# Kernel tuning notes

Measured on AMD Instinct MI355X. Metric: run time of the kernel, lower is better.

The kernel has to match this reference:

```python
import jax, jax.numpy as jnp
import numpy as np

D_MODEL, D_FF, N_EXPERTS, TOP_K = 1024, 2048, 8, 2
B, S = 2, 2048

def setup_inputs() -> dict:
    key = jax.random.key(0)
    k1, k2, k3, k4 = jax.random.split(key, 4)
    scale = 0.02
    return {
        "x": jax.random.normal(k1, (B, S, D_MODEL), dtype=jnp.float32),
        "gate_w": jax.random.normal(k2, (D_MODEL, N_EXPERTS), dtype=jnp.float32) * scale,
        "w1": jax.random.normal(k3, (N_EXPERTS, D_MODEL, D_FF), dtype=jnp.float32) * scale,
        "w2": jax.random.normal(k4, (N_EXPERTS, D_FF, D_MODEL), dtype=jnp.float32) * scale,
    }

def reference(x, gate_w, w1, w2):
    # --- Router (eval mode: no exploration noise, no dropout) ---
    router_logits = jnp.einsum('bsd,de->bse', x, gate_w)          # [B,S,E]
    top_logits, top_idx = jax.lax.top_k(router_logits, TOP_K)      # [B,S,K]
    top_w = jax.nn.softmax(top_logits, axis=-1)                    # [B,S,K]
    # topk indices are distinct per token, so per-(token,expert) combine weight
    # is the sum over k of weight_k * 1[idx_k == e] (matches torch gather/argmax logic)
    combine = jnp.sum(
        jax.nn.one_hot(top_idx, N_EXPERTS, dtype=x.dtype) * top_w[..., None],
        axis=-2)                                                   # [B,S,E]
    # --- Experts: dense-compute formulation of the gather/MLP/scatter loop ---
    h = jax.nn.silu(jnp.einsum('bsd,edf->ebsf', x, w1))            # [E,B,S,Dff]
    y = jnp.einsum('ebsf,efd->ebsd', h, w2)                        # [E,B,S,D]
    out = jnp.einsum('ebsd,bse->bsd', y, combine)                  # [B,S,D]
    return out
```

## Files before the change

### kernel.cpp

```cpp
#include <hip/hip_runtime.h>
#include <cstdint>
#include <cstddef>

#define D_MODEL 1024
#define D_FF    2048
#define N_EXP   8
#define NTOK    4096
#define NASSIGN (NTOK * 2)

typedef __bf16 bf16_t;
typedef bf16_t bf16x8 __attribute__((ext_vector_type(8)));
typedef float  f32x4  __attribute__((ext_vector_type(4)));

typedef __attribute__((address_space(3))) void       lds_void;
typedef const __attribute__((address_space(1))) void gl_void;

__device__ __forceinline__ unsigned short f2b(float f) {
  union { float f; unsigned u; } v; v.f = f;
  unsigned u = v.u;
  unsigned r = (u + 0x7FFFu + ((u >> 16) & 1u)) >> 16;
  return (unsigned short)r;
}
__device__ __forceinline__ float b2f(unsigned short b) {
  union { unsigned u; float f; } v; v.u = ((unsigned)b) << 16; return v.f;
}

__global__ __launch_bounds__(256) void router_k(
    const float* __restrict__ x, const float* __restrict__ gw,
    int* __restrict__ eidx, float* __restrict__ ewt)
{
  const int wv = threadIdx.x >> 6, lane = threadIdx.x & 63;
  const int token = blockIdx.x * 4 + wv;
  const float4* xr4 = (const float4*)(x + (size_t)token * D_MODEL);
  const float4* gw4 = (const float4*)gw;

  float acc[8] = {};
  #pragma unroll
  for (int it = 0; it < 4; ++it) {
    float4 xv = xr4[it * 64 + lane];
    int d0 = it * 256 + lane * 4;
    #pragma unroll
    for (int i = 0; i < 4; ++i) {
      int d = d0 + i;
      float4 g0 = gw4[d * 2];
      float4 g1 = gw4[d * 2 + 1];
      float xs = (i == 0) ? xv.x : (i == 1) ? xv.y : (i == 2) ? xv.z : xv.w;
      acc[0] += xs * g0.x; acc[1] += xs * g0.y;
      acc[2] += xs * g0.z; acc[3] += xs * g0.w;
      acc[4] += xs * g1.x; acc[5] += xs * g1.y;
      acc[6] += xs * g1.z; acc[7] += xs * g1.w;
    }
  }
  #pragma unroll
  for (int m = 1; m < 64; m <<= 1) {
    #pragma unroll
    for (int k = 0; k < 8; ++k) acc[k] += __shfl_xor(acc[k], m);
  }
  if (lane == 0) {
    int i1 = 0; float v1 = acc[0];
    #pragma unroll
    for (int k = 1; k < 8; ++k) if (acc[k] > v1) { v1 = acc[k]; i1 = k; }
    int i2 = -1; float v2 = -1e30f;
    #pragma unroll
    for (int k = 0; k < 8; ++k) if (k != i1 && acc[k] > v2) { v2 = acc[k]; i2 = k; }
    float t  = __expf(v2 - v1);
    float w1 = 1.f / (1.f + t);
    float w2 = t * w1;
    eidx[token * 2 + 0] = i1; eidx[token * 2 + 1] = i2;
    ewt [token * 2 + 0] = w1; ewt [token * 2 + 1] = w2;
  }
}

__global__ __launch_bounds__(256) void scan_k(
    const int* __restrict__ eidx, const float* __restrict__ ewt,
    int* __restrict__ counts, int* __restrict__ offsets,
    int* __restrict__ rowtok, float* __restrict__ rowwt, int* __restrict__ rowof)
{
  __shared__ int hist[256][9];
  __shared__ int soff[8];
  const int t = threadIdx.x;

  int local[8] = {};
  #pragma unroll 4
  for (int i = 0; i < 32; ++i) local[eidx[t * 32 + i]]++;
  #pragma unroll
  for (int e = 0; e < 8; ++e) hist[t][e] = local[e];
  __syncthreads();

  for (int ofs = 1; ofs < 256; ofs <<= 1) {
    int v[8];
    if (t >= ofs) {
      #pragma unroll
      for (int e = 0; e < 8; ++e) v[e] = hist[t - ofs][e];
    }
    __syncthreads();
    if (t >= ofs) {
      #pragma unroll
      for (int e = 0; e < 8; ++e) hist[t][e] += v[e];
    }
    __syncthreads();
  }

  if (t == 0) {
    int o = 0;
    for (int e = 0; e < 8; ++e) {
      int c = hist[255][e];
      counts[e] = c;
      offsets[e] = o;
      soff[e] = o;
      o += c;
    }
  }
  __syncthreads();

  int run[8];
  #pragma unroll
  for (int e = 0; e < 8; ++e) run[e] = soff[e] + hist[t][e] - local[e];

  #pragma unroll 4
  for (int i = 0; i < 32; ++i) {
    int b = t * 32 + i;
    int e = eidx[b];
    int row = run[e]++;
    rowtok[row] = b >> 1;
    rowwt[row]  = ewt[b];
    rowof[b]    = row;
  }
}

__global__ __launch_bounds__(256) void gather_k(
    const float* __restrict__ x, const int* __restrict__ rowtok,
    unsigned short* __restrict__ Xe)
{
  const int row = blockIdx.x;
  const int token = rowtok[row];
  const float4* xr = (const float4*)(x + (size_t)token * D_MODEL);
  ushort4* dst = (ushort4*)(Xe + (size_t)row * D_MODEL);
  float4 v = xr[threadIdx.x];
  ushort4 o;
  o.x = f2b(v.x); o.y = f2b(v.y); o.z = f2b(v.z); o.w = f2b(v.w);
  dst[threadIdx.x] = o;
}

__global__ __launch_bounds__(256) void transcvt_k(
    const float* __restrict__ in, unsigned short* __restrict__ out, int R, int C)
{
  __shared__ float T[64][65];
  const int e = blockIdx.z;
  const float* ein = in + (size_t)e * R * C;
  unsigned short* eout = out + (size_t)e * R * C;
  const int c0 = blockIdx.x * 64, r0 = blockIdx.y * 64;
  const int g = threadIdx.x >> 4;
  const int m = threadIdx.x & 15;

  #pragma unroll
  for (int i = 0; i < 4; ++i) {
    int r = i * 16 + g;
    float4 v = *(const float4*)(ein + (size_t)(r0 + r) * C + c0 + m * 4);
    T[r][m * 4 + 0] = v.x; T[r][m * 4 + 1] = v.y;
    T[r][m * 4 + 2] = v.z; T[r][m * 4 + 3] = v.w;
  }
  __syncthreads();
  #pragma unroll
  for (int i = 0; i < 4; ++i) {
    int c = i * 16 + g;
    ushort4 o;
    o.x = f2b(T[m * 4 + 0][c]); o.y = f2b(T[m * 4 + 1][c]);
    o.z = f2b(T[m * 4 + 2][c]); o.w = f2b(T[m * 4 + 3][c]);
    *(ushort4*)(eout + (size_t)(c0 + c) * R + r0 + m * 4) = o;
  }
}

template<int K, int N, int MODE>
__global__ __launch_bounds__(256) void moe_gemm_k(
    const unsigned short* __restrict__ A,
    const unsigned short* __restrict__ Bt,
    unsigned short* __restrict__ Hout,
    const int* __restrict__ counts, const int* __restrict__ offsets,
    const float* __restrict__ rowwt)
{
  const int e = blockIdx.z;
  const int cnt = counts[e];
  const int m0 = blockIdx.y * 128;
  if (m0 >= cnt) return;
  const int base = offsets[e];
  const int n0 = blockIdx.x * 128;

  __shared__ unsigned short lA[128 * 32];
  __shared__ unsigned short lB[128 * 32];

  const int tid = threadIdx.x;
  const int lane = tid & 63;
  const int wv = tid >> 6;
  const int wm = wv & 1, wn = wv >> 1;
  const int col = lane & 15, quad = lane >> 4;

  const unsigned short* Aseg = A + (size_t)base * K;
  const unsigned short* Bseg = Bt + (size_t)e * ((size_t)N * K);

  f32x4 acc[4][4] = {};

  for (int k0 = 0; k0 < K; k0 += 32) {
    __syncthreads();
    #pragma unroll
    for (int r = 0; r < 2; ++r) {
      int flat = ((r * 4 + wv) * 64 + lane) * 16;
      int row = flat >> 6;
      int kb  = flat & 63;
      const char* gA = (const char*)Aseg + ((size_t)(m0 + row) * K + k0) * 2 + kb;
      const char* gB = (const char*)Bseg + ((size_t)(n0 + row) * K + k0) * 2 + kb;
      char* lpa = (char*)lA + (r * 4 + wv) * 1024;
      char* lpb = (char*)lB + (r * 4 + wv) * 1024;
      __builtin_amdgcn_global_load_lds((gl_void*)gA, (lds_void*)lpa, 16, 0, 0);
      __builtin_amdgcn_global_load_lds((gl_void*)gB, (lds_void*)lpb, 16, 0, 0);
    }
    __syncthreads();

    bf16x8 af[4], bfr[4];
    #pragma unroll
    for (int i = 0; i < 4; ++i)
      af[i] = *(const bf16x8*)(lA + ((wm * 64 + i * 16 + col) * 32 + quad * 8));
    #pragma unroll
    for (int j = 0; j < 4; ++j)
      bfr[j] = *(const bf16x8*)(lB + ((wn * 64 + j * 16 + col) * 32 + quad * 8));
    #pragma unroll
    for (int i = 0; i < 4; ++i)
      #pragma unroll
      for (int j = 0; j < 4; ++j)
        acc[i][j] = __builtin_amdgcn_mfma_f32_16x16x32_bf16(af[i], bfr[j], acc[i][j], 0, 0, 0);
  }

  #pragma unroll
  for (int i = 0; i < 4; ++i) {
    #pragma unroll
    for (int reg = 0; reg < 4; ++reg) {
      int r = m0 + wm * 64 + i * 16 + quad * 4 + reg;
      if (r < cnt) {
        unsigned short* hrow = Hout + (size_t)(base + r) * N + (n0 + wn * 64 + col);
        if (MODE == 1) {
          #pragma unroll
          for (int j = 0; j < 4; ++j) {
            float v = acc[i][j][reg];
            float s = v / (1.f + __expf(-v));
            hrow[j * 16] = f2b(s);
          }
        } else {
          float wgt = rowwt[base + r];
          #pragma unroll
          for (int j = 0; j < 4; ++j)
            hrow[j * 16] = f2b(wgt * acc[i][j][reg]);
        }
      }
    }
  }
}

__global__ __launch_bounds__(256) void combine_k(
    const unsigned short* __restrict__ Y, const int* __restrict__ rowof,
    float* __restrict__ out)
{
  const int token = blockIdx.x;
  const int r1 = rowof[token * 2];
  const int r2 = rowof[token * 2 + 1];
  const int d4 = threadIdx.x;
  ushort4 a = *(const ushort4*)(Y + (size_t)r1 * D_MODEL + d4 * 4);
  ushort4 b = *(const ushort4*)(Y + (size_t)r2 * D_MODEL + d4 * 4);
  float4 o;
  o.x = b2f(a.x) + b2f(b.x);
  o.y = b2f(a.y) + b2f(b.y);
  o.z = b2f(a.z) + b2f(b.z);
  o.w = b2f(a.w) + b2f(b.w);
  *(float4*)(out + (size_t)token * D_MODEL + d4 * 4) = o;
}

extern "C" void kernel_launch(void* const* d_in, const int* in_sizes, int n_in,
                              void* d_out, int out_size, void* d_ws, size_t ws_size,
                              hipStream_t stream) {
  const float* x  = (const float*)d_in[0];
  const float* gw = (const float*)d_in[1];
  const float* w1 = (const float*)d_in[2];
  const float* w2 = (const float*)d_in[3];
  float* out = (float*)d_out;

  char* ws = (char*)d_ws;
  size_t off = 0;
  auto alloc = [&](size_t bytes) -> char* {
    char* p = ws + off; off += (bytes + 255) & ~(size_t)255; return p;
  };
  int*   ctrl    = (int*)alloc(256);
  int*   counts  = ctrl;
  int*   offsets = ctrl + 8;
  int*   eidx    = (int*)  alloc((size_t)NASSIGN * 4);
  float* ewt     = (float*)alloc((size_t)NASSIGN * 4);
  int*   rowtok  = (int*)  alloc((size_t)NASSIGN * 4);
  float* rowwt   = (float*)alloc((size_t)NASSIGN * 4);
  int*   rowof   = (int*)  alloc((size_t)NASSIGN * 4);
  unsigned short* Xe  = (unsigned short*)alloc((size_t)(NASSIGN + 128) * D_MODEL * 2);
  unsigned short* H   = (unsigned short*)alloc((size_t)(NASSIGN + 128) * D_FF * 2);
  unsigned short* Y   = (unsigned short*)alloc((size_t)(NASSIGN + 128) * D_MODEL * 2);
  unsigned short* w1t = (unsigned short*)alloc((size_t)N_EXP * D_MODEL * D_FF * 2);
  unsigned short* w2t = (unsigned short*)alloc((size_t)N_EXP * D_MODEL * D_FF * 2);

  router_k<<<NTOK / 4, 256, 0, stream>>>(x, gw, eidx, ewt);
  scan_k<<<1, 256, 0, stream>>>(eidx, ewt, counts, offsets, rowtok, rowwt, rowof);
  gather_k<<<NASSIGN, 256, 0, stream>>>(x, rowtok, Xe);
  transcvt_k<<<dim3(D_FF / 64, D_MODEL / 64, N_EXP), 256, 0, stream>>>(w1, w1t, D_MODEL, D_FF);
  transcvt_k<<<dim3(D_MODEL / 64, D_FF / 64, N_EXP), 256, 0, stream>>>(w2, w2t, D_FF, D_MODEL);

  moe_gemm_k<D_MODEL, D_FF, 1><<<dim3(D_FF / 128, 32, N_EXP), 256, 0, stream>>>(
      Xe, w1t, H, counts, offsets, rowwt);
  moe_gemm_k<D_FF, D_MODEL, 2><<<dim3(D_MODEL / 128, 32, N_EXP), 256, 0, stream>>>(
      H, w2t, Y, counts, offsets, rowwt);
  combine_k<<<NTOK, 256, 0, stream>>>(Y, rowof, out);
}
```

Baseline: 348.9 us.

## Fuse weight transposes into router, compact tile list, widen K tile with swizzled LDS

The router and both weight transpose-convert kernels are merged into one prep kernel, removing two launches and letting them run concurrently. The scan now writes a compact list of (expert, m0) tiles, so the grouped GEMMs launch a flat grid over real tiles instead of a 32x8 grid where most blocks exit early. The GEMM K step grows from 32 to 64 with an XOR-swizzled LDS layout to avoid bank conflicts and halve the barriers per K. LDS use doubles and MAXTILE caps the tile count at 72.

```diff
diff --git a/kernel.cpp b/kernel.cpp
--- a/kernel.cpp
+++ b/kernel.cpp
@@ -7,6 +7,7 @@
 #define N_EXP   8
 #define NTOK    4096
 #define NASSIGN (NTOK * 2)
+#define MAXTILE 72
 
 typedef __bf16 bf16_t;
 typedef bf16_t bf16x8 __attribute__((ext_vector_type(8)));
@@ -25,12 +26,59 @@
   union { unsigned u; float f; } v; v.u = ((unsigned)b) << 16; return v.f;
 }
 
-__global__ __launch_bounds__(256) void router_k(
+__device__ __forceinline__ void transpose_tile(
+    const float* __restrict__ ein, unsigned short* __restrict__ eout,
+    int R, int C, int bx, int by, float (*T)[65], int tid)
+{
+  const int c0 = bx * 64, r0 = by * 64;
+  const int g = tid >> 4;
+  const int m = tid & 15;
+  #pragma unroll
+  for (int i = 0; i < 4; ++i) {
+    int r = i * 16 + g;
+    float4 v = *(const float4*)(ein + (size_t)(r0 + r) * C + c0 + m * 4);
+    T[r][m * 4 + 0] = v.x; T[r][m * 4 + 1] = v.y;
+    T[r][m * 4 + 2] = v.z; T[r][m * 4 + 3] = v.w;
+  }
+  __syncthreads();
+  #pragma unroll
+  for (int i = 0; i < 4; ++i) {
+    int c = i * 16 + g;
+    ushort4 o;
+    o.x = f2b(T[m * 4 + 0][c]); o.y = f2b(T[m * 4 + 1][c]);
+    o.z = f2b(T[m * 4 + 2][c]); o.w = f2b(T[m * 4 + 3][c]);
+    *(ushort4*)(eout + (size_t)(c0 + c) * R + r0 + m * 4) = o;
+  }
+}
+
+__global__ __launch_bounds__(256) void prep_k(
     const float* __restrict__ x, const float* __restrict__ gw,
+    const float* __restrict__ w1, const float* __restrict__ w2,
+    unsigned short* __restrict__ w1t, unsigned short* __restrict__ w2t,
     int* __restrict__ eidx, float* __restrict__ ewt)
 {
-  const int wv = threadIdx.x >> 6, lane = threadIdx.x & 63;
-  const int token = blockIdx.x * 4 + wv;
+  __shared__ float T[64][65];
+  const int bid = blockIdx.x;
+  const int tid = threadIdx.x;
+
+  if (bid < 4096) {
+    int bx = bid & 31, by = (bid >> 5) & 15, e = bid >> 9;
+    transpose_tile(w1 + (size_t)e * D_MODEL * D_FF,
+                   w1t + (size_t)e * D_MODEL * D_FF,
+                   D_MODEL, D_FF, bx, by, T, tid);
+    return;
+  }
+  if (bid < 8192) {
+    int b = bid - 4096;
+    int bx = b & 15, by = (b >> 4) & 31, e = b >> 9;
+    transpose_tile(w2 + (size_t)e * D_MODEL * D_FF,
+                   w2t + (size_t)e * D_MODEL * D_FF,
+                   D_FF, D_MODEL, bx, by, T, tid);
+    return;
+  }
+  const int rb = bid - 8192;
+  const int wv = tid >> 6, lane = tid & 63;
+  const int token = rb * 4 + wv;
   const float4* xr4 = (const float4*)(x + (size_t)token * D_MODEL);
   const float4* gw4 = (const float4*)gw;
 
@@ -64,17 +112,18 @@
     #pragma unroll
     for (int k = 0; k < 8; ++k) if (k != i1 && acc[k] > v2) { v2 = acc[k]; i2 = k; }
     float t  = __expf(v2 - v1);
-    float w1 = 1.f / (1.f + t);
-    float w2 = t * w1;
+    float wa = 1.f / (1.f + t);
+    float wb = t * wa;
     eidx[token * 2 + 0] = i1; eidx[token * 2 + 1] = i2;
-    ewt [token * 2 + 0] = w1; ewt [token * 2 + 1] = w2;
+    ewt [token * 2 + 0] = wa; ewt [token * 2 + 1] = wb;
   }
 }
 
 __global__ __launch_bounds__(256) void scan_k(
     const int* __restrict__ eidx, const float* __restrict__ ewt,
     int* __restrict__ counts, int* __restrict__ offsets,
-    int* __restrict__ rowtok, float* __restrict__ rowwt, int* __restrict__ rowof)
+    int* __restrict__ rowtok, float* __restrict__ rowwt, int* __restrict__ rowof,
+    int* __restrict__ tile_e, int* __restrict__ tile_m0, int* __restrict__ tile_n)
 {
   __shared__ int hist[256][9];
   __shared__ int soff[8];
@@ -102,14 +151,17 @@
   }
 
   if (t == 0) {
-    int o = 0;
+    int o = 0, tt = 0;
     for (int e = 0; e < 8; ++e) {
       int c = hist[255][e];
       counts[e] = c;
       offsets[e] = o;
       soff[e] = o;
+      int nt = (c + 127) >> 7;
+      for (int i = 0; i < nt; ++i) { tile_e[tt] = e; tile_m0[tt] = i * 128; ++tt; }
       o += c;
     }
+    tile_n[0] = tt;
   }
   __syncthreads();
 
@@ -142,52 +194,26 @@
   dst[threadIdx.x] = o;
 }
 
-__global__ __launch_bounds__(256) void transcvt_k(
-    const float* __restrict__ in, unsigned short* __restrict__ out, int R, int C)
-{
-  __shared__ float T[64][65];
-  const int e = blockIdx.z;
-  const float* ein = in + (size_t)e * R * C;
-  unsigned short* eout = out + (size_t)e * R * C;
-  const int c0 = blockIdx.x * 64, r0 = blockIdx.y * 64;
-  const int g = threadIdx.x >> 4;
-  const int m = threadIdx.x & 15;
-
-  #pragma unroll
-  for (int i = 0; i < 4; ++i) {
-    int r = i * 16 + g;
-    float4 v = *(const float4*)(ein + (size_t)(r0 + r) * C + c0 + m * 4);
-    T[r][m * 4 + 0] = v.x; T[r][m * 4 + 1] = v.y;
-    T[r][m * 4 + 2] = v.z; T[r][m * 4 + 3] = v.w;
-  }
-  __syncthreads();
-  #pragma unroll
-  for (int i = 0; i < 4; ++i) {
-    int c = i * 16 + g;
-    ushort4 o;
-    o.x = f2b(T[m * 4 + 0][c]); o.y = f2b(T[m * 4 + 1][c]);
-    o.z = f2b(T[m * 4 + 2][c]); o.w = f2b(T[m * 4 + 3][c]);
-    *(ushort4*)(eout + (size_t)(c0 + c) * R + r0 + m * 4) = o;
-  }
-}
-
-template<int K, int N, int MODE>
+template<int K, int N, int NT_LOG2, int MODE>
 __global__ __launch_bounds__(256) void moe_gemm_k(
     const unsigned short* __restrict__ A,
     const unsigned short* __restrict__ Bt,
     unsigned short* __restrict__ Hout,
     const int* __restrict__ counts, const int* __restrict__ offsets,
-    const float* __restrict__ rowwt)
-{
-  const int e = blockIdx.z;
+    const float* __restrict__ rowwt,
+    const int* __restrict__ tile_e, const int* __restrict__ tile_m0,
+    const int* __restrict__ tile_n)
+{
+  const int t = blockIdx.x >> NT_LOG2;
+  if (t >= tile_n[0]) return;
+  const int e   = tile_e[t];
+  const int m0  = tile_m0[t];
+  const int n0  = (blockIdx.x & ((1 << NT_LOG2) - 1)) * 128;
   const int cnt = counts[e];
-  const int m0 = blockIdx.y * 128;
-  if (m0 >= cnt) return;
   const int base = offsets[e];
-  const int n0 = blockIdx.x * 128;
-
-  __shared__ unsigned short lA[128 * 32];
-  __shared__ unsigned short lB[128 * 32];
+
+  __shared__ unsigned short lA[128 * 64];
+  __shared__ unsigned short lB[128 * 64];
 
   const int tid = threadIdx.x;
   const int lane = tid & 63;
@@ -198,36 +224,45 @@
   const unsigned short* Aseg = A + (size_t)base * K;
   const unsigned short* Bseg = Bt + (size_t)e * ((size_t)N * K);
 
+  const int lrow = lane >> 3;
+  const int gch  = (lane & 7) ^ lrow;
+
   f32x4 acc[4][4] = {};
 
-  for (int k0 = 0; k0 < K; k0 += 32) {
+  for (int k0 = 0; k0 < K; k0 += 64) {
     __syncthreads();
     #pragma unroll
-    for (int r = 0; r < 2; ++r) {
-      int flat = ((r * 4 + wv) * 64 + lane) * 16;
-      int row = flat >> 6;
-      int kb  = flat & 63;
-      const char* gA = (const char*)Aseg + ((size_t)(m0 + row) * K + k0) * 2 + kb;
-      const char* gB = (const char*)Bseg + ((size_t)(n0 + row) * K + k0) * 2 + kb;
-      char* lpa = (char*)lA + (r * 4 + wv) * 1024;
-      char* lpb = (char*)lB + (r * 4 + wv) * 1024;
-      __builtin_amdgcn_global_load_lds((gl_void*)gA, (lds_void*)lpa, 16, 0, 0);
-      __builtin_amdgcn_global_load_lds((gl_void*)gB, (lds_void*)lpb, 16, 0, 0);
+    for (int r = 0; r < 4; ++r) {
+      int s = r * 4 + wv;
+      int row = s * 8 + lrow;
+      const char* gA = (const char*)Aseg + ((size_t)(m0 + row) * K + k0) * 2 + gch * 16;
+      const char* gB = (const char*)Bseg + ((size_t)(n0 + row) * K + k0) * 2 + gch * 16;
+      __builtin_amdgcn_global_load_lds((gl_void*)gA, (lds_void*)((char*)lA + s * 1024), 16, 0, 0);
+      __builtin_amdgcn_global_load_lds((gl_void*)gB, (lds_void*)((char*)lB + s * 1024), 16, 0, 0);
     }
     __syncthreads();
 
-    bf16x8 af[4], bfr[4];
-    #pragma unroll
-    for (int i = 0; i < 4; ++i)
-      af[i] = *(const bf16x8*)(lA + ((wm * 64 + i * 16 + col) * 32 + quad * 8));
-    #pragma unroll
-    for (int j = 0; j < 4; ++j)
-      bfr[j] = *(const bf16x8*)(lB + ((wn * 64 + j * 16 + col) * 32 + quad * 8));
-    #pragma unroll
-    for (int i = 0; i < 4; ++i)
-      #pragma unroll
-      for (int j = 0; j < 4; ++j)
-        acc[i][j] = __builtin_amdgcn_mfma_f32_16x16x32_bf16(af[i], bfr[j], acc[i][j], 0, 0, 0);
+    #pragma unroll
+    for (int kk = 0; kk < 2; ++kk) {
+      bf16x8 af[4], bfr[4];
+      #pragma unroll
+      for (int i = 0; i < 4; ++i) {
+        int r = wm * 64 + i * 16 + col;
+        int p = ((kk << 2) | quad) ^ (col & 7);
+        af[i] = *(const bf16x8*)(lA + r * 64 + p * 8);
+      }
+      #pragma unroll
+      for (int j = 0; j < 4; ++j) {
+        int r = wn * 64 + j * 16 + col;
+        int p = ((kk << 2) | quad) ^ (col & 7);
+        bfr[j] = *(const bf16x8*)(lB + r * 64 + p * 8);
+      }
+      #pragma unroll
+      for (int i = 0; i < 4; ++i)
+        #pragma unroll
+        for (int j = 0; j < 4; ++j)
+          acc[i][j] = __builtin_amdgcn_mfma_f32_16x16x32_bf16(af[i], bfr[j], acc[i][j], 0, 0, 0);
+    }
   }
 
   #pragma unroll
@@ -287,9 +322,12 @@
   auto alloc = [&](size_t bytes) -> char* {
     char* p = ws + off; off += (bytes + 255) & ~(size_t)255; return p;
   };
-  int*   ctrl    = (int*)alloc(256);
+  int*   ctrl    = (int*)alloc(1024);
   int*   counts  = ctrl;
   int*   offsets = ctrl + 8;
+  int*   tile_n  = ctrl + 16;
+  int*   tile_e  = ctrl + 32;
+  int*   tile_m0 = ctrl + 32 + MAXTILE;
   int*   eidx    = (int*)  alloc((size_t)NASSIGN * 4);
   float* ewt     = (float*)alloc((size_t)NASSIGN * 4);
   int*   rowtok  = (int*)  alloc((size_t)NASSIGN * 4);
@@ -301,15 +339,14 @@
   unsigned short* w1t = (unsigned short*)alloc((size_t)N_EXP * D_MODEL * D_FF * 2);
   unsigned short* w2t = (unsigned short*)alloc((size_t)N_EXP * D_MODEL * D_FF * 2);
 
-  router_k<<<NTOK / 4, 256, 0, stream>>>(x, gw, eidx, ewt);
-  scan_k<<<1, 256, 0, stream>>>(eidx, ewt, counts, offsets, rowtok, rowwt, rowof);
+  prep_k<<<8192 + NTOK / 4, 256, 0, stream>>>(x, gw, w1, w2, w1t, w2t, eidx, ewt);
+  scan_k<<<1, 256, 0, stream>>>(eidx, ewt, counts, offsets, rowtok, rowwt, rowof,
+                                tile_e, tile_m0, tile_n);
   gather_k<<<NASSIGN, 256, 0, stream>>>(x, rowtok, Xe);
-  transcvt_k<<<dim3(D_FF / 64, D_MODEL / 64, N_EXP), 256, 0, stream>>>(w1, w1t, D_MODEL, D_FF);
-  transcvt_k<<<dim3(D_MODEL / 64, D_FF / 64, N_EXP), 256, 0, stream>>>(w2, w2t, D_FF, D_MODEL);
-
-  moe_gemm_k<D_MODEL, D_FF, 1><<<dim3(D_FF / 128, 32, N_EXP), 256, 0, stream>>>(
-      Xe, w1t, H, counts, offsets, rowwt);
-  moe_gemm_k<D_FF, D_MODEL, 2><<<dim3(D_MODEL / 128, 32, N_EXP), 256, 0, stream>>>(
-      H, w2t, Y, counts, offsets, rowwt);
+
+  moe_gemm_k<D_MODEL, D_FF, 4, 1><<<MAXTILE * 16, 256, 0, stream>>>(
+      Xe, w1t, H, counts, offsets, rowwt, tile_e, tile_m0, tile_n);
+  moe_gemm_k<D_FF, D_MODEL, 3, 2><<<MAXTILE * 8, 256, 0, stream>>>(
+      H, w2t, Y, counts, offsets, rowwt, tile_e, tile_m0, tile_n);
   combine_k<<<NTOK, 256, 0, stream>>>(Y, rowof, out);
 }
```

Result: slower. 379.2 us (+8.7%).
